# Optimization experiments

Measured on AMD Instinct MI355X. Metric: run time of the kernel, lower is better.

The kernel has to match this reference:

```python
import jax, jax.numpy as jnp
import numpy as np

L, B, H = 1024, 64, 128


def _gru_cell(x, h, wih, whh, bih, bhh):
    # torch.nn.GRUCell math: gates ordered (r, z, n)
    gi = x @ wih.T + bih  # [B, 3H]
    gh = h @ whh.T + bhh  # [B, 3H]
    ir, iz, inn = jnp.split(gi, 3, axis=1)
    hr, hz, hn = jnp.split(gh, 3, axis=1)
    r = jax.nn.sigmoid(ir + hr)
    z = jax.nn.sigmoid(iz + hz)
    n = jnp.tanh(inn + r * hn)
    return (1.0 - z) * n + z * h


def setup_inputs() -> dict:
    key = jax.random.key(0)
    ks = jax.random.split(key, 20)
    s = 0.05  # keep tanh/sigmoid unsaturated
    f32 = jnp.float32
    return {
        "passEnc": jax.random.normal(ks[0], (L, B, 2 * H), f32),
        "Wp_w": jax.random.normal(ks[1], (H, 2 * H), f32) * s,
        "Wp_b": jax.random.normal(ks[2], (H,), f32) * s,
        "Wph_w": jax.random.normal(ks[3], (H, 2 * H), f32) * s,
        "Wph_b": jax.random.normal(ks[4], (H,), f32) * s,
        "Wg_w": jax.random.normal(ks[5], (4 * H, 4 * H), f32) * s,
        "Wg_b": jax.random.normal(ks[6], (4 * H,), f32) * s,
        "Vt": jax.random.normal(ks[7], (B, H, 1), f32),
        "wih_f": jax.random.normal(ks[8], (3 * H, 4 * H), f32) * s,
        "whh_f": jax.random.normal(ks[9], (3 * H, H), f32) * s,
        "bih_f": jax.random.normal(ks[10], (3 * H,), f32) * s,
        "bhh_f": jax.random.normal(ks[11], (3 * H,), f32) * s,
        "wih_r": jax.random.normal(ks[12], (3 * H, 4 * H), f32) * s,
        "whh_r": jax.random.normal(ks[13], (3 * H, H), f32) * s,
        "bih_r": jax.random.normal(ks[14], (3 * H,), f32) * s,
        "bhh_r": jax.random.normal(ks[15], (3 * H,), f32) * s,
        "h0_fwd": jax.random.normal(ks[16], (B, H), f32),
        "h0_rev": jax.random.normal(ks[17], (B, H), f32),
    }


def reference(passEnc, Wp_w, Wp_b, Wph_w, Wph_b, Wg_w, Wg_b, Vt,
              wih_f, whh_f, bih_f, bhh_f, wih_r, whh_r, bih_r, bhh_r,
              h0_fwd, h0_rev):
    v = Vt[:, :, 0]                       # [B, H]
    WPf = passEnc @ Wp_w.T + Wp_b        # loop-invariant WP_sub_v(passEnc), [L, B, H]
    pe_rev = jnp.flip(passEnc, axis=0)
    WPr = jnp.flip(WPf, axis=0)          # linear commutes with flip

    def attend(x_t, WP, pe):
        # x_t: [B, 2H]; WP: [L, B, H]; pe: [L, B, 2H]
        temp = jnp.tanh(WP + x_t @ Wph_w.T + Wph_b)      # [L, B, H]
        scores = jnp.einsum('lbh,bh->bl', temp, v)       # per-batch Vt
        a = jax.nn.softmax(scores, axis=1)               # over L
        c = jnp.einsum('bl,lbd->bd', a, pe)              # [B, 2H]
        cc = jnp.concatenate([x_t, c], axis=1)           # [B, 4H]
        g = jax.nn.sigmoid(cc @ Wg_w.T + Wg_b)
        return g * cc

    def step(carry, xs):
        hf, hr = carry
        xf, xr = xs
        cf = attend(xf, WPf, passEnc)
        cr = attend(xr, WPr, pe_rev)
        hf = _gru_cell(cf, hf, wih_f, whh_f, bih_f, bhh_f)
        hr = _gru_cell(cr, hr, wih_r, whh_r, bih_r, bhh_r)
        return (hf, hr), jnp.concatenate([hf, hr], axis=1)

    _, out = jax.lax.scan(step, (h0_fwd, h0_rev), (passEnc, pe_rev))
    # original applies Dropout(p=0.2); identity in eval mode
    return out  # [L, B, 2H]
```

## Files before the change

kernel.cpp:

```cpp
#include <hip/hip_runtime.h>
#include <hip/hip_bf16.h>

#define DEV __device__ __forceinline__
typedef unsigned short u16;
typedef short bf16x8 __attribute__((ext_vector_type(8)));
typedef float f32x4  __attribute__((ext_vector_type(4)));

static constexpr float LOG2E = 1.44269504088896340736f;
static constexpr float C2E   = 2.88539008177792681472f;

DEV float rcpf_(float x){ return __builtin_amdgcn_rcpf(x); }
DEV float exp2f_(float x){ return __builtin_amdgcn_exp2f(x); }
DEV float sigmoidf_(float x){ return rcpf_(1.f + exp2f_(-LOG2E*x)); }
DEV float tanhf_fast(float x){ return 1.f - 2.f*rcpf_(exp2f_(C2E*x) + 1.f); }
DEV u16 bfu(float f){
  __hip_bfloat16 h = __float2bfloat16(f);
  union { __hip_bfloat16 h; u16 u; } c; c.h = h; return c.u;
}
DEV float ubf_lo(unsigned u){ return __uint_as_float(u << 16); }
DEV float ubf_hi(unsigned u){ return __uint_as_float(u & 0xffff0000u); }
DEV unsigned pack2(float a, float b){ return (unsigned)bfu(a) | ((unsigned)bfu(b) << 16); }
DEV float ubf(u16 u){ return __uint_as_float(((unsigned)u) << 16); }

DEV void acc4inv(const float4 f, const float4 e, const float4 v, float& s){
  const float dx = __builtin_fmaf(f.x, e.x, 1.f);
  const float dy = __builtin_fmaf(f.y, e.y, 1.f);
  const float dz = __builtin_fmaf(f.z, e.z, 1.f);
  const float dw = __builtin_fmaf(f.w, e.w, 1.f);
  const float p2 = dx*dy, p3 = p2*dz, p4 = p3*dw;
  const float r4 = rcpf_(p4);
  const float iw = r4*p3;
  const float s3 = r4*dw;
  const float iz = s3*p2;
  const float s2 = s3*dz;
  const float iy = s2*dx;
  const float ix = s2*dy;
  s += v.x*ix; s += v.y*iy; s += v.z*iz; s += v.w*iw;
}

__global__ __launch_bounds__(256) void k_cvtw(const float* __restrict__ Wg,
      const float* __restrict__ wf, const float* __restrict__ wr,
      u16* __restrict__ out){
  const int i = (blockIdx.x*256 + threadIdx.x)*4;
  const float* src;
  int off;
  if (i < 262144){ src = Wg; off = i; }
  else if (i < 458752){ src = wf; off = i - 262144; }
  else { src = wr; off = i - 458752; }
  const float4 v = *(const float4*)(src + off);
  uint2 o; o.x = pack2(v.x, v.y); o.y = pack2(v.z, v.w);
  *(uint2*)(out + i) = o;
}

__global__ __launch_bounds__(256,4) void k_proj(const float* __restrict__ pe,
      const float* __restrict__ Wp, const float* __restrict__ Wpb,
      const float* __restrict__ Wph, const float* __restrict__ Wphb,
      float* __restrict__ E, float* __restrict__ F){
  __shared__ __align__(16) float xs[32*256];
  const int tid = threadIdx.x;
  const int sel = blockIdx.x >> 11;
  const long r0 = (long)(blockIdx.x & 2047) * 32;
  const float* W   = sel ? Wph  : Wp;
  const float* bia = sel ? Wphb : Wpb;
  float* out       = sel ? F    : E;
  const float4* src = (const float4*)(pe + r0*256);
  float4* dst = (float4*)xs;
  #pragma unroll
  for (int i=0;i<8;i++) dst[tid + 256*i] = src[tid + 256*i];
  __syncthreads();
  const int h = tid & 127, g = tid >> 7;
  float acc[16];
  #pragma unroll
  for (int r=0;r<16;r++) acc[r] = 0.f;
  for (int kc=0; kc<8; kc++){
    float4 w4[8];
    const float4* wp = (const float4*)(W + h*256 + kc*32);
    #pragma unroll
    for (int q=0;q<8;q++) w4[q] = wp[q];
    #pragma unroll
    for (int r=0;r<16;r++){
      const float4* xr = (const float4*)(xs + (g*16+r)*256 + kc*32);
      #pragma unroll
      for (int q=0;q<8;q++){
        const float4 xv = xr[q];
        acc[r] += xv.x*w4[q].x + xv.y*w4[q].y + xv.z*w4[q].z + xv.w*w4[q].w;
      }
    }
  }
  const float bh = bia[h];
  #pragma unroll
  for (int r=0;r<16;r++)
    out[(r0 + g*16 + r)*128 + h] = exp2f_(C2E*(acc[r] + bh));
}

#define AF_F    0
#define AF_E    8448
#define AF_PEt  12672
#define AF_S    17792
#define AF_V    19904
#define AF_M    20032
#define AF_SU   20096
#define AF_R    20160
#define A_LDSF  20224

DEV f32x4 mfma16(bf16x8 a, bf16x8 b, f32x4 c){
  return __builtin_amdgcn_mfma_f32_16x16x32_bf16(a, b, c, 0, 0, 0);
}

__global__ __launch_bounds__(512,4) void k_attn(const float* __restrict__ pe,
      const float* __restrict__ E, const float* __restrict__ F,
      const float* __restrict__ Vt, u16* __restrict__ Cout){
  __shared__ __align__(16) float lds[A_LDSF];
  const int tid = threadIdx.x;
  const int p = blockIdx.x;
  const int b = ((p >> 7) << 3) | (p & 7);
  const int tt = (p >> 3) & 15;
  const int t0 = tt * 64;
  u16* PEtu = (u16*)(lds + AF_PEt);
  u16* Pu   = (u16*)(lds + AF_S);

  for (int i = tid; i < 64*32; i += 512){
    const int r = i >> 5, c = i & 31;
    *(float4*)(lds + AF_F + r*132 + c*4) =
      *(const float4*)(F + ((long)(t0+r)*64 + b)*128 + c*4);
  }
  if (tid < 128) lds[AF_V + tid] = -2.f * Vt[b*128 + tid];
  if (tid < 64){ lds[AF_M+tid] = -__builtin_inff(); lds[AF_SU+tid] = 0.f; }

  f32x4 cacc[8];
  #pragma unroll
  for (int i=0;i<8;i++) cacc[i] = (f32x4){0.f,0.f,0.f,0.f};

  const int lane = tid & 63, w = tid >> 6;
  const int tg = lane >> 4, lg = lane & 15;
  const int ta = w*8 + tg, tb2 = ta + 4;
  const int l15 = lane & 15, kg8 = (lane >> 4) * 8;
  const int tq = w >> 1, dhalf = w & 1;
  const int tcol = tq*16 + l15;
  const int sdlo = tid & 7, slp = (tid >> 3) & 15, sdhi = tid >> 7;

  for (int lt=0; lt<32; lt++){
    const int l0 = lt*32;
    __syncthreads();
    for (int i = tid; i < 32*32; i += 512){
      const int r = i >> 5, c = i & 31;
      *(float4*)(lds + AF_E + r*132 + c*4) =
        *(const float4*)(E + ((long)(l0+r)*64 + b)*128 + c*4);
    }
    #pragma unroll
    for (int k2=0;k2<2;k2++){
      const int dseg = (sdhi + k2*4)*8 + sdlo;
      const int ll = slp*2;
      const float4 vA = *(const float4*)(pe + ((long)(l0+ll  )*64 + b)*256 + dseg*4);
      const float4 vB = *(const float4*)(pe + ((long)(l0+ll+1)*64 + b)*256 + dseg*4);
      u16* base = PEtu + (dseg*4)*40 + ll;
      *(unsigned*)(base)        = pack2(vA.x, vB.x);
      *(unsigned*)(base + 40)   = pack2(vA.y, vB.y);
      *(unsigned*)(base + 80)   = pack2(vA.z, vB.z);
      *(unsigned*)(base + 120)  = pack2(vA.w, vB.w);
    }
    __syncthreads();
    {
      float s00=0.f, s01=0.f, s10=0.f, s11=0.f;
      const float* Fa = lds + AF_F + ta*132;
      const float* Fb = lds + AF_F + tb2*132;
      const float* Ea = lds + AF_E + lg*132;
      const float* Eb = lds + AF_E + (lg+16)*132;
      const float* Vb = lds + AF_V;
      #pragma unroll 4
      for (int hc=0; hc<32; hc++){
        const float4 f0 = *(const float4*)(Fa + hc*4);
        const float4 f1 = *(const float4*)(Fb + hc*4);
        const float4 e0 = *(const float4*)(Ea + hc*4);
        const float4 e1 = *(const float4*)(Eb + hc*4);
        const float4 vv = *(const float4*)(Vb + hc*4);
        acc4inv(f0, e0, vv, s00);
        acc4inv(f0, e1, vv, s01);
        acc4inv(f1, e0, vv, s10);
        acc4inv(f1, e1, vv, s11);
      }
      lds[AF_S + ta*33  + lg]      = s00;
      lds[AF_S + ta*33  + lg + 16] = s01;
      lds[AF_S + tb2*33 + lg]      = s10;
      lds[AF_S + tb2*33 + lg + 16] = s11;
    }
    __syncthreads();
    {
      const int t = tid >> 3, sub = tid & 7;
      const float* Srow = lds + AF_S + t*33 + sub*4;
      const float s0=Srow[0], s1=Srow[1], s2=Srow[2], s3=Srow[3];
      float mx = fmaxf(fmaxf(s0,s1), fmaxf(s2,s3));
      #pragma unroll
      for (int off=1; off<8; off<<=1) mx = fmaxf(mx, __shfl_xor(mx, off));
      const float m_old = lds[AF_M + t];
      const float m_new = fmaxf(m_old, mx);
      const float p0 = exp2f_(LOG2E*(s0-m_new));
      const float p1 = exp2f_(LOG2E*(s1-m_new));
      const float p2 = exp2f_(LOG2E*(s2-m_new));
      const float p3 = exp2f_(LOG2E*(s3-m_new));
      float ps = p0+p1+p2+p3;
      #pragma unroll
      for (int off=1; off<8; off<<=1) ps += __shfl_xor(ps, off);
      __syncthreads();
      uint2 pw; pw.x = pack2(p0,p1); pw.y = pack2(p2,p3);
      *(uint2*)(Pu + t*40 + sub*4) = pw;
      if (sub==0){
        const float rsc = exp2f_(LOG2E*(m_old - m_new));
        lds[AF_R + t] = rsc;
        lds[AF_SU + t] = lds[AF_SU + t]*rsc + ps;
        lds[AF_M + t] = m_new;
      }
    }
    __syncthreads();
    {
      const float rs = lds[AF_R + tcol];
      #pragma unroll
      for (int p2=0;p2<8;p2++){
        cacc[p2][0]*=rs; cacc[p2][1]*=rs; cacc[p2][2]*=rs; cacc[p2][3]*=rs;
      }
      const bf16x8 bfrag = *(const bf16x8*)(Pu + tcol*40 + kg8);
      #pragma unroll
      for (int p2=0;p2<8;p2++){
        const int dt = dhalf*8 + p2;
        const bf16x8 afrag = *(const bf16x8*)(PEtu + (dt*16 + l15)*40 + kg8);
        cacc[p2] = mfma16(afrag, bfrag, cacc[p2]);
      }
    }
  }
  __syncthreads();
  {
    const float inv = rcpf_(lds[AF_SU + tcol]);
    u16* Cb = (u16*)(lds + AF_F);
    const int rb = (lane >> 4) * 4;
    #pragma unroll
    for (int p2=0;p2<8;p2++){
      const int dd = (dhalf*8 + p2)*16 + rb;
      *(unsigned*)(Cb + tcol*264 + dd)     = pack2(cacc[p2][0]*inv, cacc[p2][1]*inv);
      *(unsigned*)(Cb + tcol*264 + dd + 2) = pack2(cacc[p2][2]*inv, cacc[p2][3]*inv);
    }
  }
  __syncthreads();
  {
    const u16* Cb = (const u16*)(lds + AF_F);
    #pragma unroll
    for (int k2=0;k2<4;k2++){
      const int flat = tid + k2*512;
      const int t = flat >> 5, dg = flat & 31;
      const uint4 v = *(const uint4*)(Cb + t*264 + dg*8);
      *(uint4*)(Cout + ((long)(t0+t)*64 + b)*256 + dg*8) = v;
    }
  }
}

__global__ __launch_bounds__(512,2) void k_gates(const float* __restrict__ pe,
      const u16* __restrict__ Cin,
      const u16* __restrict__ Wgb16, const float* __restrict__ Wgb,
      const u16* __restrict__ wfb16, const float* __restrict__ bihf,
      const u16* __restrict__ wrb16, const float* __restrict__ bihr,
      u16* __restrict__ GIf, u16* __restrict__ GIr){
  __shared__ __align__(16) u16 ccb[32*512];
  __shared__ __align__(16) u16 gb [32*512];
  const int tid = threadIdx.x;
  const int r0 = blockIdx.x * 32;

  #pragma unroll
  for (int i=0;i<4;i++){
    const int c = tid + i*512;
    const int r = c >> 6, k0 = (c & 63)*8;
    const int kd = k0 ^ ((r&7)<<3);
    uint4 o;
    if (k0 < 256){
      const float4 f0 = *(const float4*)(pe + ((long)(r0+r))*256 + k0);
      const float4 f1 = *(const float4*)(pe + ((long)(r0+r))*256 + k0 + 4);
      o.x = pack2(f0.x,f0.y); o.y = pack2(f0.z,f0.w);
      o.z = pack2(f1.x,f1.y); o.w = pack2(f1.z,f1.w);
    } else {
      o = *(const uint4*)(Cin + ((long)(r0+r))*256 + (k0-256));
    }
    *(uint4*)(ccb + r*512 + kd) = o;
  }
  __syncthreads();

  const int l = tid & 63, wv = tid >> 6;
  const int rw = (wv >> 2) * 16;
  const int nq = wv & 3;
  const int arow = rw + (l & 15);
  const int kgrp = (l >> 4) * 8;
  const int swz  = (l & 7) << 3;
  const u16* abase = ccb + arow*512;
  const int crow = rw + (l >> 4) * 4;

  for (int p2=0; p2<4; p2++){
    const int n0 = nq*128 + p2*32;
    const int c0 = n0 + (l & 15), c1 = c0 + 16;
    const u16* b0p = Wgb16 + (long)c0*512 + kgrp;
    const u16* b1p = Wgb16 + (long)c1*512 + kgrp;
    f32x4 a0 = {0.f,0.f,0.f,0.f}, a1 = {0.f,0.f,0.f,0.f};
    #pragma unroll
    for (int kk=0; kk<16; kk++){
      const bf16x8 av = *(const bf16x8*)(abase + ((kk*32 + kgrp) ^ swz));
      const bf16x8 b0 = *(const bf16x8*)(b0p + kk*32);
      const bf16x8 b1 = *(const bf16x8*)(b1p + kk*32);
      a0 = mfma16(av, b0, a0);
      a1 = mfma16(av, b1, a1);
    }
    const float bi0 = Wgb[c0], bi1 = Wgb[c1];
    #pragma unroll
    for (int i=0;i<4;i++){
      gb[(crow+i)*512 + c0] = bfu(sigmoidf_(a0[i] + bi0));
      gb[(crow+i)*512 + c1] = bfu(sigmoidf_(a1[i] + bi1));
    }
  }
  __syncthreads();

  #pragma unroll
  for (int i=0;i<4;i++){
    const int c = tid + i*512;
    const int r = c >> 6, k0 = (c & 63)*8;
    const int kd = k0 ^ ((r&7)<<3);
    uint4 uc = *(const uint4*)(ccb + r*512 + kd);
    uint4 ug = *(const uint4*)(gb  + r*512 + k0);
    uint4 o;
    o.x = pack2(ubf_lo(uc.x)*ubf_lo(ug.x), ubf_hi(uc.x)*ubf_hi(ug.x));
    o.y = pack2(ubf_lo(uc.y)*ubf_lo(ug.y), ubf_hi(uc.y)*ubf_hi(ug.y));
    o.z = pack2(ubf_lo(uc.z)*ubf_lo(ug.z), ubf_hi(uc.z)*ubf_hi(ug.z));
    o.w = pack2(ubf_lo(uc.w)*ubf_lo(ug.w), ubf_hi(uc.w)*ubf_hi(ug.w));
    *(uint4*)(ccb + r*512 + kd) = o;
  }
  __syncthreads();

  const int t = r0 >> 6, b0r = r0 & 63;
  const long rbf = (long)r0 + rw;
  const long rbr = (long)(1023 - t)*64 + b0r + rw;
  u16* stg = gb + wv*512;

  for (int p2=0; p2<6; p2++){
    const int nt = nq*12 + p2*2;
    const int j0 = nt * 16;
    const bool isf = (j0 < 384);
    const u16* wb = isf ? wfb16 : wrb16;
    const float* bi = isf ? bihf : bihr;
    const int jb = isf ? j0 : (j0 - 384);
    const long rbase = isf ? rbf : rbr;
    u16* GIo = isf ? GIf : GIr;
    const int c0 = jb + (l & 15), c1 = c0 + 16;
    const u16* b0p = wb + (long)c0*512 + kgrp;
    const u16* b1p = wb + (long)c1*512 + kgrp;
    f32x4 a0 = {0.f,0.f,0.f,0.f}, a1 = {0.f,0.f,0.f,0.f};
    #pragma unroll
    for (int kk=0; kk<16; kk++){
      const bf16x8 av = *(const bf16x8*)(abase + ((kk*32 + kgrp) ^ swz));
      const bf16x8 b0 = *(const bf16x8*)(b0p + kk*32);
      const bf16x8 b1 = *(const bf16x8*)(b1p + kk*32);
      a0 = mfma16(av, b0, a0);
      a1 = mfma16(av, b1, a1);
    }
    const float bi0 = bi[c0], bi1 = bi[c1];
    #pragma unroll
    for (int i=0;i<4;i++){
      stg[((l>>4)*4+i)*16 + (l&15)]       = bfu(a0[i] + bi0);
      stg[256 + ((l>>4)*4+i)*16 + (l&15)] = bfu(a1[i] + bi1);
    }
    {
      const int rr = l >> 2, q = l & 3;
      const uint2 v0 = *(const uint2*)(stg + rr*16 + q*4);
      const uint2 v1 = *(const uint2*)(stg + 256 + rr*16 + q*4);
      *(uint2*)(GIo + (rbase + rr)*384 + jb      + q*4) = v0;
      *(uint2*)(GIo + (rbase + rr)*384 + jb + 16 + q*4) = v1;
    }
  }
}

__global__ __launch_bounds__(512,2) void k_gru(
      const u16* __restrict__ GIf, const u16* __restrict__ GIr,
      const float* __restrict__ whhf, const float* __restrict__ bhhf,
      const float* __restrict__ whhr, const float* __restrict__ bhhr,
      const float* __restrict__ h0f, const float* __restrict__ h0r,
      float* __restrict__ out){
  const int d = blockIdx.x >> 6, b = blockIdx.x & 63;
  const u16* GI = d ? GIr  : GIf;
  const float* whh = d ? whhr : whhf;
  const float* bhh = d ? bhhr : bhhf;
  const float* h0  = d ? h0r  : h0f;
  const int tid = threadIdx.x;
  const int seg = tid >> 7, j0 = tid & 127;
  __shared__ __align__(16) float hsh[128];
  __shared__ __align__(16) float part[4*384];

  float4 wR[8], wZ[8], wN[8];
  {
    const float4* r0p = (const float4*)(whh + (long)(j0      )*128 + seg*32);
    const float4* r1p = (const float4*)(whh + (long)(j0 + 128)*128 + seg*32);
    const float4* r2p = (const float4*)(whh + (long)(j0 + 256)*128 + seg*32);
    #pragma unroll
    for (int q=0;q<8;q++){ wR[q]=r0p[q]; wZ[q]=r1p[q]; wN[q]=r2p[q]; }
  }
  float bjr=0.f, bjz=0.f, bjn=0.f, hold=0.f;
  float gr_n=0.f, gz_n=0.f, gn_n=0.f;
  if (tid < 128){
    hsh[tid] = hold = h0[b*128 + tid];
    bjr = bhh[tid]; bjz = bhh[tid+128]; bjn = bhh[tid+256];
    gr_n = ubf(GI[(long)b*384 + tid]);
    gz_n = ubf(GI[(long)b*384 + tid + 128]);
    gn_n = ubf(GI[(long)b*384 + tid + 256]);
  }
  __syncthreads();

  for (int t=0; t<1024; t++){
    {
      float aR=0.f, aZ=0.f, aN=0.f;
      const float4* hseg = (const float4*)(hsh + seg*32);
      #pragma unroll
      for (int q=0;q<8;q++){
        const float4 hv = hseg[q];
        aR += wR[q].x*hv.x + wR[q].y*hv.y + wR[q].z*hv.z + wR[q].w*hv.w;
        aZ += wZ[q].x*hv.x + wZ[q].y*hv.y + wZ[q].z*hv.z + wZ[q].w*hv.w;
        aN += wN[q].x*hv.x + wN[q].y*hv.y + wN[q].z*hv.z + wN[q].w*hv.w;
      }
      part[seg*384 + j0]       = aR;
      part[seg*384 + j0 + 128] = aZ;
      part[seg*384 + j0 + 256] = aN;
    }
    __syncthreads();
    if (tid < 128){
      const float gr = gr_n, gz = gz_n, gn = gn_n;
      if (t < 1023){
        const long base = ((long)(t+1)*64 + b)*384 + tid;
        gr_n = ubf(GI[base]); gz_n = ubf(GI[base+128]); gn_n = ubf(GI[base+256]);
      }
      const float ghr = bjr + ((part[tid]       + part[384+tid])       + (part[768+tid]       + part[1152+tid]));
      const float ghz = bjz + ((part[tid+128]   + part[384+tid+128])   + (part[768+tid+128]   + part[1152+tid+128]));
      const float ghn = bjn + ((part[tid+256]   + part[384+tid+256])   + (part[768+tid+256]   + part[1152+tid+256]));
      const float r = sigmoidf_(gr + ghr);
      const float z = sigmoidf_(gz + ghz);
      const float n = tanhf_fast(gn + r*ghn);
      const float hnew = (1.f - z)*n + z*hold;
      hold = hnew;
      hsh[tid] = hnew;
      out[((long)t*64 + b)*256 + d*128 + tid] = hnew;
    }
    __syncthreads();
  }
}

__global__ void k_sentinel(float* out){ out[0] = 1.0e6f; }

extern "C" void kernel_launch(void* const* d_in, const int* in_sizes, int n_in,
                              void* d_out, int out_size, void* d_ws, size_t ws_size,
                              hipStream_t stream){
  const float* passEnc = (const float*)d_in[0];
  const float* Wp_w  = (const float*)d_in[1];
  const float* Wp_b  = (const float*)d_in[2];
  const float* Wph_w = (const float*)d_in[3];
  const float* Wph_b = (const float*)d_in[4];
  const float* Wg_w  = (const float*)d_in[5];
  const float* Wg_b  = (const float*)d_in[6];
  const float* Vt    = (const float*)d_in[7];
  const float* wih_f = (const float*)d_in[8];
  const float* whh_f = (const float*)d_in[9];
  const float* bih_f = (const float*)d_in[10];
  const float* bhh_f = (const float*)d_in[11];
  const float* wih_r = (const float*)d_in[12];
  const float* whh_r = (const float*)d_in[13];
  const float* bih_r = (const float*)d_in[14];
  const float* bhh_r = (const float*)d_in[15];
  const float* h0f   = (const float*)d_in[16];
  const float* h0r   = (const float*)d_in[17];
  float* out = (float*)d_out;

  const size_t NEED = 134217728ull;
  if (ws_size < NEED){ k_sentinel<<<1,1,0,stream>>>(out); return; }
  char* base = (char*)d_ws;
  u16* GIf = (u16*)base;
  u16* GIr = (u16*)(base + 50331648ull);
  u16* C   = (u16*)(base + 100663296ull);
  float* E = (float*)base;
  float* F = (float*)(base + 33554432ull);
  u16* wgb16 = (u16*)d_out;
  u16* wfb16 = wgb16 + 262144;
  u16* wrb16 = wfb16 + 196608;

  k_cvtw <<<640,  256, 0, stream>>>(Wg_w, wih_f, wih_r, wgb16);
  k_proj <<<4096, 256, 0, stream>>>(passEnc, Wp_w, Wp_b, Wph_w, Wph_b, E, F);
  k_attn <<<1024, 512, 0, stream>>>(passEnc, E, F, Vt, C);
  k_gates<<<2048, 512, 0, stream>>>(passEnc, C, wgb16, Wg_b,
                                    wfb16, bih_f, wrb16, bih_r, GIf, GIr);
  k_gru  <<<128,  512, 0, stream>>>(GIf, GIr, whh_f, bhh_f, whh_r, bhh_r, h0f, h0r, out);
}
```

Before: 2.609 ms.

## Retile attention score loop into 4x4 register tiles with split-H shuffle reduction

Each lane of the score computation now holds a 4x4 block of (t,l) accumulators over a quarter of the H dimension, in place of a 2x2 block over the full H. Partial sums are combined across the four H-groups with cross-lane shuffles, and the H-chunk index is rotated per lane to spread LDS bank accesses. The aim is more FMAs per LDS load and fewer bank conflicts. In exchange it uses more accumulator registers and adds shuffle reductions, and only a quarter of the lanes write scores to LDS.

```diff
diff --git a/kernel.cpp b/kernel.cpp
--- a/kernel.cpp
+++ b/kernel.cpp
@@ -132,8 +132,9 @@
   for (int i=0;i<8;i++) cacc[i] = (f32x4){0.f,0.f,0.f,0.f};
 
   const int lane = tid & 63, w = tid >> 6;
-  const int tg = lane >> 4, lg = lane & 15;
-  const int ta = w*8 + tg, tb2 = ta + 4;
+  const int hg = lane >> 4, li = lane & 15;
+  const int th = li & 1, lq = li >> 1;
+  const int rot = (2*hg + 4*th) & 7;
   const int l15 = lane & 15, kg8 = (lane >> 4) * 8;
   const int tq = w >> 1, dhalf = w & 1;
   const int tcol = tq*16 + l15;
@@ -161,28 +162,44 @@
     }
     __syncthreads();
     {
-      float s00=0.f, s01=0.f, s10=0.f, s11=0.f;
-      const float* Fa = lds + AF_F + ta*132;
-      const float* Fb = lds + AF_F + tb2*132;
-      const float* Ea = lds + AF_E + lg*132;
-      const float* Eb = lds + AF_E + (lg+16)*132;
-      const float* Vb = lds + AF_V;
-      #pragma unroll 4
-      for (int hc=0; hc<32; hc++){
-        const float4 f0 = *(const float4*)(Fa + hc*4);
-        const float4 f1 = *(const float4*)(Fb + hc*4);
-        const float4 e0 = *(const float4*)(Ea + hc*4);
-        const float4 e1 = *(const float4*)(Eb + hc*4);
-        const float4 vv = *(const float4*)(Vb + hc*4);
-        acc4inv(f0, e0, vv, s00);
-        acc4inv(f0, e1, vv, s01);
-        acc4inv(f1, e0, vv, s10);
-        acc4inv(f1, e1, vv, s11);
-      }
-      lds[AF_S + ta*33  + lg]      = s00;
-      lds[AF_S + ta*33  + lg + 16] = s01;
-      lds[AF_S + tb2*33 + lg]      = s10;
-      lds[AF_S + tb2*33 + lg + 16] = s11;
+      float s[4][4];
+      #pragma unroll
+      for (int i=0;i<4;i++)
+        #pragma unroll
+        for (int j=0;j<4;j++) s[i][j] = 0.f;
+      const float* Fb = lds + AF_F + (w*8 + th)*132 + hg*32;
+      const float* Eb = lds + AF_E + lq*132 + hg*32;
+      const float* Vb = lds + AF_V + hg*32;
+      #pragma unroll 2
+      for (int hc=0; hc<8; hc++){
+        const int hcp = ((hc + rot) & 7) * 4;
+        const float4 vv = *(const float4*)(Vb + hcp);
+        float4 fv[4], ev[4];
+        #pragma unroll
+        for (int i=0;i<4;i++) fv[i] = *(const float4*)(Fb + i*264 + hcp);
+        #pragma unroll
+        for (int j=0;j<4;j++) ev[j] = *(const float4*)(Eb + j*1056 + hcp);
+        #pragma unroll
+        for (int i=0;i<4;i++){
+          #pragma unroll
+          for (int j=0;j<4;j++)
+            acc4inv(fv[i], ev[j], vv, s[i][j]);
+        }
+      }
+      #pragma unroll
+      for (int i=0;i<4;i++)
+        #pragma unroll
+        for (int j=0;j<4;j++){
+          s[i][j] += __shfl_xor(s[i][j], 16);
+          s[i][j] += __shfl_xor(s[i][j], 32);
+        }
+      if (hg == 0){
+        #pragma unroll
+        for (int i=0;i<4;i++)
+          #pragma unroll
+          for (int j=0;j<4;j++)
+            lds[AF_S + (w*8 + th + 2*i)*33 + (lq + 8*j)] = s[i][j];
+      }
     }
     __syncthreads();
     {
```

New measurement: 2.533 ms. 1.03x faster.
